# Optimization experiments

Hardware: AMD Instinct MI355X
Metric: run time of the kernel (lower is better)

The kernel has to match this reference:

```python
import jax, jax.numpy as jnp
import numpy as np

N_ROI = 262144
FEATURE_DIM = 256
HIDDEN_DIM = 64
N_NETWORKS = 128


def setup_inputs() -> dict:
    key = jax.random.key(0)
    ks = jax.random.split(key, 5)
    x = jax.random.normal(ks[0], (N_ROI, FEATURE_DIM), dtype=jnp.float32)
    group = jax.random.randint(ks[1], (N_ROI,), 0, N_NETWORKS, dtype=jnp.int32)
    W1 = jax.random.normal(ks[2], (FEATURE_DIM, HIDDEN_DIM), dtype=jnp.float32) / np.sqrt(FEATURE_DIM)
    b1 = jnp.zeros((HIDDEN_DIM,), dtype=jnp.float32)
    W2 = jax.random.normal(ks[3], (HIDDEN_DIM, 1), dtype=jnp.float32) / np.sqrt(HIDDEN_DIM)
    b2 = jnp.zeros((1,), dtype=jnp.float32)
    return {"x": x, "group": group, "W1": W1, "b1": b1, "W2": W2, "b2": b2}


def reference(x, group, W1, b1, W2, b2):
    # attention MLP score per ROI: Linear -> ReLU -> Linear(->1)
    h = jax.nn.relu(x @ W1 + b1)                       # [N, H]
    score = (h @ W2)[:, 0] + b2[0]                     # [N]
    # numerically-stable segment softmax over each network's ROIs
    seg_max = jax.ops.segment_max(score, group, num_segments=N_NETWORKS)  # [K]
    seg_max = jnp.where(jnp.isfinite(seg_max), seg_max, 0.0)              # empty segments -> 0
    w = jnp.exp(score - seg_max[group])                # [N] unnormalized weights
    denom = jax.ops.segment_sum(w, group, num_segments=N_NETWORKS)        # [K]
    num = jax.ops.segment_sum(w[:, None] * x, group, num_segments=N_NETWORKS)  # [K, D]
    # empty networks produce zeros (matches torch.zeros_like branch)
    return jnp.where(denom[:, None] > 0, num / jnp.maximum(denom, 1e-30)[:, None], 0.0)
```

## Files before the change

kernel.cpp:

```cpp
#include <hip/hip_runtime.h>
#include <hip/hip_bf16.h>

#define N_ROI 262144
#define FDIM  256
#define HDIM  64
#define NNET  128

#define TILE   128
#define TILES  8
#define RPB    (TILE * TILES)
#define NBLK   (N_ROI / RPB)
#define XPITCH 264

typedef __attribute__((ext_vector_type(8))) __bf16 bf16x8;
typedef __attribute__((ext_vector_type(8))) short short8;
typedef __attribute__((ext_vector_type(4))) float floatx4;

union frag_cast { short8 s; bf16x8 b; };

#define NEG_INF (-__builtin_huge_valf())

__device__ __forceinline__ unsigned fkey(float f) {
  unsigned u = __float_as_uint(f);
  return (u & 0x80000000u) ? ~u : (u | 0x80000000u);
}
__device__ __forceinline__ float fkey_inv(unsigned k) {
  unsigned u = (k & 0x80000000u) ? (k ^ 0x80000000u) : ~k;
  return __uint_as_float(u);
}
__device__ __forceinline__ unsigned short f2bf(float f) {
  unsigned u = __float_as_uint(f);
  u += 0x7FFFu + ((u >> 16) & 1u);
  return (unsigned short)(u >> 16);
}
__device__ __forceinline__ float bf2f(unsigned short h) {
  return __uint_as_float(((unsigned)h) << 16);
}
__device__ __forceinline__ unsigned cvt2(float a, float b) {
  union { __hip_bfloat162 h; unsigned u; } cv;
  cv.h = __float22bfloat162_rn(make_float2(a, b));
  return cv.u;
}

__global__ __launch_bounds__(512, 2) void fused_kernel(
    const float* __restrict__ x, const int* __restrict__ group,
    const float* __restrict__ W1, const float* __restrict__ b1,
    const float* __restrict__ W2,
    float* __restrict__ num_ws,
    float* __restrict__ m_ws)
{
  __shared__ __align__(16) unsigned short w1t[HDIM][XPITCH];
  __shared__ __align__(16) unsigned short xl[TILE][XPITCH];
  __shared__ float sc[TILE];
  __shared__ int   ggrp[TILE];
  __shared__ unsigned gw[TILE];
  __shared__ unsigned tmax[NNET];
  __shared__ __align__(16) float fl[NNET];
  __shared__ float mrun[NNET];
  __shared__ float dent[NNET];
  __shared__ float denrun[NNET];

  const int tid  = threadIdx.x;
  const int wave = tid >> 6, lane = tid & 63;
  const int col  = lane & 15, quad = lane >> 4;

  {
    const int n = tid & 63, kg = tid >> 6;
    for (int p = 0; p < 4; ++p) {
      const int k0 = p * 64 + kg * 8;
      unsigned short tmp[8];
#pragma unroll
      for (int j = 0; j < 8; ++j) tmp[j] = f2bf(W1[(k0 + j) * HDIM + n]);
      *(short8*)&w1t[n][k0] = *(short8*)tmp;
    }
  }
  if (tid < NNET) { mrun[tid] = NEG_INF; denrun[tid] = 0.f; }

  float b1v[4], w2v[4];
#pragma unroll
  for (int nt = 0; nt < 4; ++nt) { b1v[nt] = b1[nt * 16 + col]; w2v[nt] = W2[nt * 16 + col]; }

  floatx4 acc[8][2];
#pragma unroll
  for (int mt = 0; mt < 8; ++mt) { acc[mt][0] = (floatx4)0.f; acc[mt][1] = (floatx4)0.f; }

  const size_t rbase = (size_t)blockIdx.x * RPB;
  const float* xb = x + rbase * FDIM;

  float4 pf[16];
#pragma unroll
  for (int i = 0; i < 16; ++i)
    pf[i] = *(const float4*)(xb + i * 2048 + tid * 4);

  for (int t = 0; t < TILES; ++t) {
    __syncthreads();
#pragma unroll
    for (int i = 0; i < 16; ++i) {
      const int row = i * 8 + (tid >> 6);
      const int dim = (tid & 63) * 4;
      unsigned lo = cvt2(pf[i].x, pf[i].y);
      unsigned hi = cvt2(pf[i].z, pf[i].w);
      uint2 pk; pk.x = lo; pk.y = hi;
      *(uint2*)&xl[row][dim] = pk;
    }
    if (tid < TILE) {
      ggrp[tid] = group[rbase + t * TILE + tid];
      tmax[tid] = 0u;
      dent[tid] = 0.f;
    }
    __syncthreads();

    if (t < TILES - 1) {
      const float* xn = xb + (size_t)(t + 1) * TILE * FDIM;
#pragma unroll
      for (int i = 0; i < 16; ++i)
        pf[i] = *(const float4*)(xn + i * 2048 + tid * 4);
    }

    floatx4 accS[4];
#pragma unroll
    for (int nt = 0; nt < 4; ++nt) accS[nt] = (floatx4)0.f;
#pragma unroll
    for (int c = 0; c < 8; ++c) {
      frag_cast af;
      af.s = *(const short8*)&xl[wave * 16 + col][c * 32 + quad * 8];
#pragma unroll
      for (int nt = 0; nt < 4; ++nt) {
        frag_cast bf;
        bf.s = *(const short8*)&w1t[nt * 16 + col][c * 32 + quad * 8];
        accS[nt] = __builtin_amdgcn_mfma_f32_16x16x32_bf16(af.b, bf.b, accS[nt], 0, 0, 0);
      }
    }
    {
      float pr[4];
#pragma unroll
      for (int r = 0; r < 4; ++r) pr[r] = 0.f;
#pragma unroll
      for (int nt = 0; nt < 4; ++nt)
#pragma unroll
        for (int r = 0; r < 4; ++r)
          pr[r] += fmaxf(accS[nt][r] + b1v[nt], 0.f) * w2v[nt];
#pragma unroll
      for (int off = 1; off < 16; off <<= 1)
#pragma unroll
        for (int r = 0; r < 4; ++r) pr[r] += __shfl_xor(pr[r], off, 16);
      if (col == 0) {
#pragma unroll
        for (int r = 0; r < 4; ++r) sc[wave * 16 + quad * 4 + r] = pr[r];
      }
    }
    __syncthreads();

    if (tid < TILE) atomicMax(&tmax[ggrp[tid]], fkey(sc[tid]));
    __syncthreads();
    if (tid < NNET) {
      const unsigned tk = tmax[tid];
      float f = 1.f;
      if (tk) {
        const float mo = mrun[tid];
        const float mn = fmaxf(mo, fkey_inv(tk));
        f = __expf(mo - mn);
        mrun[tid] = mn;
      }
      fl[tid] = f;
    }
    __syncthreads();
    if (tid < TILE) {
      const int g = ggrp[tid];
      const float w = __expf(sc[tid] - mrun[g]);
      const unsigned short wb = f2bf(w);
      gw[tid] = ((unsigned)ggrp[tid] << 16) | wb;
      atomicAdd(&dent[g], bf2f(wb));
    }
#pragma unroll
    for (int mt = 0; mt < 8; ++mt) {
      const floatx4 f4 = *(const floatx4*)&fl[mt * 16 + quad * 4];
#pragma unroll
      for (int r = 0; r < 4; ++r) {
        acc[mt][0][r] *= f4[r];
        acc[mt][1][r] *= f4[r];
      }
    }
    __syncthreads();
    if (tid < NNET) denrun[tid] = denrun[tid] * fl[tid] + dent[tid];

    const int ntb = wave * 32;
#pragma unroll
    for (int c = 0; c < 4; ++c) {
      unsigned gwv[8];
#pragma unroll
      for (int j = 0; j < 8; ++j) gwv[j] = gw[c * 32 + quad * 8 + j];
      frag_cast bfx[2];
#pragma unroll
      for (int nt = 0; nt < 2; ++nt) {
        unsigned short bb[8];
#pragma unroll
        for (int j = 0; j < 8; ++j)
          bb[j] = xl[c * 32 + quad * 8 + j][ntb + nt * 16 + col];
        bfx[nt].s = *(short8*)bb;
      }
#pragma unroll
      for (int mt = 0; mt < 8; ++mt) {
        const unsigned gt = (unsigned)(mt * 16 + col);
        unsigned short aa[8];
#pragma unroll
        for (int j = 0; j < 8; ++j)
          aa[j] = ((gwv[j] >> 16) == gt) ? (unsigned short)gwv[j] : (unsigned short)0;
        frag_cast af; af.s = *(short8*)aa;
        acc[mt][0] = __builtin_amdgcn_mfma_f32_16x16x32_bf16(af.b, bfx[0].b, acc[mt][0], 0, 0, 0);
        acc[mt][1] = __builtin_amdgcn_mfma_f32_16x16x32_bf16(af.b, bfx[1].b, acc[mt][1], 0, 0, 0);
      }
    }
  }

  float* slice = num_ws + (size_t)blockIdx.x * (NNET * 257);
#pragma unroll
  for (int mt = 0; mt < 8; ++mt)
#pragma unroll
    for (int nt = 0; nt < 2; ++nt)
#pragma unroll
      for (int r = 0; r < 4; ++r)
        slice[(mt * 16 + quad * 4 + r) * 257 + wave * 32 + nt * 16 + col] = acc[mt][nt][r];
  if (tid < NNET) {
    slice[tid * 257 + 256] = denrun[tid];
    m_ws[(size_t)blockIdx.x * NNET + tid] = mrun[tid];
  }
}

__global__ __launch_bounds__(256) void finalize_kernel(
    const float* __restrict__ num_ws, const float* __restrict__ m_ws,
    float* __restrict__ out)
{
  const int g = blockIdx.x;
  const int tid = threadIdx.x;
  __shared__ float e_l[NBLK];
  __shared__ float dsum[NBLK];
  __shared__ float wm[4];

  const float mb = m_ws[(size_t)tid * NNET + g];
  float M = mb;
#pragma unroll
  for (int off = 1; off < 64; off <<= 1) M = fmaxf(M, __shfl_xor(M, off));
  if ((tid & 63) == 0) wm[tid >> 6] = M;
  __syncthreads();
  M = fmaxf(fmaxf(wm[0], wm[1]), fmaxf(wm[2], wm[3]));

  const float eb = (mb == NEG_INF) ? 0.f : __expf(mb - M);
  const float db = num_ws[(size_t)tid * (NNET * 257) + g * 257 + 256];
  e_l[tid]  = eb;
  dsum[tid] = db * eb;
  __syncthreads();

  float num = 0.f, den = 0.f;
#pragma unroll 4
  for (int b = 0; b < NBLK; ++b) {
    num += num_ws[(size_t)b * (NNET * 257) + g * 257 + tid] * e_l[b];
    den += dsum[b];
  }
  out[g * FDIM + tid] = (den > 0.f) ? num / fmaxf(den, 1e-30f) : 0.f;
}

extern "C" void kernel_launch(void* const* d_in, const int* in_sizes, int n_in,
                              void* d_out, int out_size, void* d_ws, size_t ws_size,
                              hipStream_t stream)
{
  const float* x     = (const float*)d_in[0];
  const int*   group = (const int*)d_in[1];
  const float* W1    = (const float*)d_in[2];
  const float* b1    = (const float*)d_in[3];
  const float* W2    = (const float*)d_in[4];
  float* out = (float*)d_out;

  float* num_ws = (float*)d_ws;
  float* m_ws   = num_ws + (size_t)NBLK * NNET * 257;

  fused_kernel<<<NBLK, 512, 0, stream>>>(x, group, W1, b1, W2, num_ws, m_ws);
  finalize_kernel<<<NNET, 256, 0, stream>>>(num_ws, m_ws, out);

  (void)in_sizes; (void)n_in; (void)out_size; (void)ws_size;
}
```

Measured before the change: 401.1 us.

## Restructure fused kernel to 256-thread blocks with 32-row chunks and swizzled LDS

The fused kernel now uses 256 threads per block over 512 rows in 16 chunks of 32. The first GEMM is split across waves by hidden column, with partial scores summed through shared memory. An XOR swizzle is applied to the x tile in LDS to reduce bank conflicts, and group ids are preloaded once per block. The block count doubles to 512, so the finalize kernel is split into two halves per network with a two-way block reduction. This trades more blocks and workspace traffic for lower per-block latency and better occupancy, but adds more barriers per row processed.

```diff
diff --git a/kernel.cpp b/kernel.cpp
--- a/kernel.cpp
+++ b/kernel.cpp
@@ -6,9 +6,9 @@
 #define HDIM  64
 #define NNET  128
 
-#define TILE   128
-#define TILES  8
-#define RPB    (TILE * TILES)
+#define CHUNK  32
+#define NCHUNK 16
+#define RPB    (CHUNK * NCHUNK)
 #define NBLK   (N_ROI / RPB)
 #define XPITCH 264
 
@@ -41,24 +41,26 @@
   cv.h = __float22bfloat162_rn(make_float2(a, b));
   return cv.u;
 }
-
-__global__ __launch_bounds__(512, 2) void fused_kernel(
+__device__ __forceinline__ int sidx(int row, int s) {
+  return row * XPITCH + (s ^ (((row >> 3) & 3) << 4));
+}
+
+__global__ __launch_bounds__(256, 2) void fused_kernel(
     const float* __restrict__ x, const int* __restrict__ group,
     const float* __restrict__ W1, const float* __restrict__ b1,
     const float* __restrict__ W2,
     float* __restrict__ num_ws,
     float* __restrict__ m_ws)
 {
-  __shared__ __align__(16) unsigned short w1t[HDIM][XPITCH];
-  __shared__ __align__(16) unsigned short xl[TILE][XPITCH];
-  __shared__ float sc[TILE];
-  __shared__ int   ggrp[TILE];
-  __shared__ unsigned gw[TILE];
+  __shared__ unsigned short w1t[HDIM][XPITCH];
+  __shared__ __align__(16) unsigned short xl[CHUNK * XPITCH];
+  __shared__ float scpart[4][CHUNK];
+  __shared__ float sc[CHUNK];
+  __shared__ int   ggrp[RPB];
+  __shared__ unsigned gw[CHUNK];
   __shared__ unsigned tmax[NNET];
   __shared__ __align__(16) float fl[NNET];
-  __shared__ float mrun[NNET];
-  __shared__ float dent[NNET];
-  __shared__ float denrun[NNET];
+  __shared__ float mrun[NNET], dent[NNET], denrun[NNET];
 
   const int tid  = threadIdx.x;
   const int wave = tid >> 6, lane = tid & 63;
@@ -66,8 +68,8 @@
 
   {
     const int n = tid & 63, kg = tid >> 6;
-    for (int p = 0; p < 4; ++p) {
-      const int k0 = p * 64 + kg * 8;
+    for (int p = 0; p < 8; ++p) {
+      const int k0 = p * 32 + kg * 8;
       unsigned short tmp[8];
 #pragma unroll
       for (int j = 0; j < 8; ++j) tmp[j] = f2bf(W1[(k0 + j) * HDIM + n]);
@@ -76,82 +78,77 @@
   }
   if (tid < NNET) { mrun[tid] = NEG_INF; denrun[tid] = 0.f; }
 
-  float b1v[4], w2v[4];
-#pragma unroll
-  for (int nt = 0; nt < 4; ++nt) { b1v[nt] = b1[nt * 16 + col]; w2v[nt] = W2[nt * 16 + col]; }
-
-  floatx4 acc[8][2];
-#pragma unroll
-  for (int mt = 0; mt < 8; ++mt) { acc[mt][0] = (floatx4)0.f; acc[mt][1] = (floatx4)0.f; }
-
   const size_t rbase = (size_t)blockIdx.x * RPB;
+  ggrp[tid]       = group[rbase + tid];
+  ggrp[tid + 256] = group[rbase + tid + 256];
+
+  const float b1s = b1[wave * 16 + col];
+  const float w2s = W2[wave * 16 + col];
+
+  floatx4 acc[8][4];
+#pragma unroll
+  for (int mt = 0; mt < 8; ++mt)
+#pragma unroll
+    for (int nt = 0; nt < 4; ++nt) acc[mt][nt] = (floatx4)0.f;
+
   const float* xb = x + rbase * FDIM;
 
-  float4 pf[16];
-#pragma unroll
-  for (int i = 0; i < 16; ++i)
-    pf[i] = *(const float4*)(xb + i * 2048 + tid * 4);
-
-  for (int t = 0; t < TILES; ++t) {
-    __syncthreads();
-#pragma unroll
-    for (int i = 0; i < 16; ++i) {
-      const int row = i * 8 + (tid >> 6);
-      const int dim = (tid & 63) * 4;
-      unsigned lo = cvt2(pf[i].x, pf[i].y);
-      unsigned hi = cvt2(pf[i].z, pf[i].w);
-      uint2 pk; pk.x = lo; pk.y = hi;
-      *(uint2*)&xl[row][dim] = pk;
-    }
-    if (tid < TILE) {
-      ggrp[tid] = group[rbase + t * TILE + tid];
-      tmax[tid] = 0u;
-      dent[tid] = 0.f;
-    }
-    __syncthreads();
-
-    if (t < TILES - 1) {
-      const float* xn = xb + (size_t)(t + 1) * TILE * FDIM;
-#pragma unroll
-      for (int i = 0; i < 16; ++i)
-        pf[i] = *(const float4*)(xn + i * 2048 + tid * 4);
-    }
-
-    floatx4 accS[4];
-#pragma unroll
-    for (int nt = 0; nt < 4; ++nt) accS[nt] = (floatx4)0.f;
+  float4 pf[8];
+#pragma unroll
+  for (int i = 0; i < 8; ++i)
+    pf[i] = *(const float4*)(xb + i * 1024 + tid * 4);
+
+  for (int ch = 0; ch < NCHUNK; ++ch) {
+    __syncthreads();
+#pragma unroll
+    for (int i = 0; i < 8; ++i) {
+      const int row = i * 4 + wave;
+      uint2 pk; pk.x = cvt2(pf[i].x, pf[i].y); pk.y = cvt2(pf[i].z, pf[i].w);
+      *(uint2*)&xl[sidx(row, lane * 4)] = pk;
+    }
+    if (tid < NNET) tmax[tid] = 0u;
+    __syncthreads();
+
+    if (ch < NCHUNK - 1) {
+      const float* xn = xb + (size_t)(ch + 1) * CHUNK * FDIM;
+#pragma unroll
+      for (int i = 0; i < 8; ++i)
+        pf[i] = *(const float4*)(xn + i * 1024 + tid * 4);
+    }
+
+    floatx4 accS[2];
+    accS[0] = (floatx4)0.f; accS[1] = (floatx4)0.f;
 #pragma unroll
     for (int c = 0; c < 8; ++c) {
-      frag_cast af;
-      af.s = *(const short8*)&xl[wave * 16 + col][c * 32 + quad * 8];
-#pragma unroll
-      for (int nt = 0; nt < 4; ++nt) {
-        frag_cast bf;
-        bf.s = *(const short8*)&w1t[nt * 16 + col][c * 32 + quad * 8];
-        accS[nt] = __builtin_amdgcn_mfma_f32_16x16x32_bf16(af.b, bf.b, accS[nt], 0, 0, 0);
+      frag_cast bw;
+      bw.s = *(const short8*)&w1t[wave * 16 + col][c * 32 + quad * 8];
+#pragma unroll
+      for (int mt = 0; mt < 2; ++mt) {
+        frag_cast af;
+        af.s = *(const short8*)&xl[sidx(mt * 16 + col, c * 32 + quad * 8)];
+        accS[mt] = __builtin_amdgcn_mfma_f32_16x16x32_bf16(af.b, bw.b, accS[mt], 0, 0, 0);
       }
     }
-    {
+#pragma unroll
+    for (int mt = 0; mt < 2; ++mt) {
       float pr[4];
 #pragma unroll
-      for (int r = 0; r < 4; ++r) pr[r] = 0.f;
-#pragma unroll
-      for (int nt = 0; nt < 4; ++nt)
-#pragma unroll
-        for (int r = 0; r < 4; ++r)
-          pr[r] += fmaxf(accS[nt][r] + b1v[nt], 0.f) * w2v[nt];
+      for (int r = 0; r < 4; ++r) pr[r] = fmaxf(accS[mt][r] + b1s, 0.f) * w2s;
 #pragma unroll
       for (int off = 1; off < 16; off <<= 1)
 #pragma unroll
         for (int r = 0; r < 4; ++r) pr[r] += __shfl_xor(pr[r], off, 16);
       if (col == 0) {
 #pragma unroll
-        for (int r = 0; r < 4; ++r) sc[wave * 16 + quad * 4 + r] = pr[r];
+        for (int r = 0; r < 4; ++r) scpart[wave][mt * 16 + quad * 4 + r] = pr[r];
       }
     }
     __syncthreads();
-
-    if (tid < TILE) atomicMax(&tmax[ggrp[tid]], fkey(sc[tid]));
+    if (tid < CHUNK) {
+      const float s = scpart[0][tid] + scpart[1][tid] + scpart[2][tid] + scpart[3][tid];
+      sc[tid] = s;
+      atomicMax(&tmax[ggrp[ch * CHUNK + tid]], fkey(s));
+    }
     __syncthreads();
     if (tid < NNET) {
       const unsigned tk = tmax[tid];
@@ -163,64 +160,61 @@
         mrun[tid] = mn;
       }
       fl[tid] = f;
-    }
-    __syncthreads();
-    if (tid < TILE) {
-      const int g = ggrp[tid];
+      dent[tid] = 0.f;
+    }
+    __syncthreads();
+    if (tid < CHUNK) {
+      const int g = ggrp[ch * CHUNK + tid];
       const float w = __expf(sc[tid] - mrun[g]);
       const unsigned short wb = f2bf(w);
-      gw[tid] = ((unsigned)ggrp[tid] << 16) | wb;
+      gw[tid] = ((unsigned)g << 16) | wb;
       atomicAdd(&dent[g], bf2f(wb));
     }
 #pragma unroll
     for (int mt = 0; mt < 8; ++mt) {
       const floatx4 f4 = *(const floatx4*)&fl[mt * 16 + quad * 4];
 #pragma unroll
-      for (int r = 0; r < 4; ++r) {
-        acc[mt][0][r] *= f4[r];
-        acc[mt][1][r] *= f4[r];
-      }
-    }
-    __syncthreads();
+      for (int nt = 0; nt < 4; ++nt)
+#pragma unroll
+        for (int r = 0; r < 4; ++r) acc[mt][nt][r] *= f4[r];
+    }
+    __syncthreads();
+
+    unsigned gwv[8];
+#pragma unroll
+    for (int j = 0; j < 8; ++j) gwv[j] = gw[quad * 8 + j];
+    frag_cast bfx[4];
+#pragma unroll
+    for (int nt = 0; nt < 4; ++nt) {
+      unsigned short bb[8];
+#pragma unroll
+      for (int j = 0; j < 8; ++j)
+        bb[j] = xl[sidx(quad * 8 + j, wave * 64 + nt * 16 + col)];
+      bfx[nt].s = *(short8*)bb;
+    }
+#pragma unroll
+    for (int mt = 0; mt < 8; ++mt) {
+      const unsigned gt = (unsigned)(mt * 16 + col);
+      unsigned short aa[8];
+#pragma unroll
+      for (int j = 0; j < 8; ++j)
+        aa[j] = ((gwv[j] >> 16) == gt) ? (unsigned short)gwv[j] : (unsigned short)0;
+      frag_cast af; af.s = *(short8*)aa;
+#pragma unroll
+      for (int nt = 0; nt < 4; ++nt)
+        acc[mt][nt] = __builtin_amdgcn_mfma_f32_16x16x32_bf16(af.b, bfx[nt].b, acc[mt][nt], 0, 0, 0);
+    }
     if (tid < NNET) denrun[tid] = denrun[tid] * fl[tid] + dent[tid];
-
-    const int ntb = wave * 32;
-#pragma unroll
-    for (int c = 0; c < 4; ++c) {
-      unsigned gwv[8];
-#pragma unroll
-      for (int j = 0; j < 8; ++j) gwv[j] = gw[c * 32 + quad * 8 + j];
-      frag_cast bfx[2];
-#pragma unroll
-      for (int nt = 0; nt < 2; ++nt) {
-        unsigned short bb[8];
-#pragma unroll
-        for (int j = 0; j < 8; ++j)
-          bb[j] = xl[c * 32 + quad * 8 + j][ntb + nt * 16 + col];
-        bfx[nt].s = *(short8*)bb;
-      }
-#pragma unroll
-      for (int mt = 0; mt < 8; ++mt) {
-        const unsigned gt = (unsigned)(mt * 16 + col);
-        unsigned short aa[8];
-#pragma unroll
-        for (int j = 0; j < 8; ++j)
-          aa[j] = ((gwv[j] >> 16) == gt) ? (unsigned short)gwv[j] : (unsigned short)0;
-        frag_cast af; af.s = *(short8*)aa;
-        acc[mt][0] = __builtin_amdgcn_mfma_f32_16x16x32_bf16(af.b, bfx[0].b, acc[mt][0], 0, 0, 0);
-        acc[mt][1] = __builtin_amdgcn_mfma_f32_16x16x32_bf16(af.b, bfx[1].b, acc[mt][1], 0, 0, 0);
-      }
-    }
   }
 
   float* slice = num_ws + (size_t)blockIdx.x * (NNET * 257);
 #pragma unroll
   for (int mt = 0; mt < 8; ++mt)
 #pragma unroll
-    for (int nt = 0; nt < 2; ++nt)
+    for (int nt = 0; nt < 4; ++nt)
 #pragma unroll
       for (int r = 0; r < 4; ++r)
-        slice[(mt * 16 + quad * 4 + r) * 257 + wave * 32 + nt * 16 + col] = acc[mt][nt][r];
+        slice[(mt * 16 + quad * 4 + r) * 257 + wave * 64 + nt * 16 + col] = acc[mt][nt][r];
   if (tid < NNET) {
     slice[tid * 257 + 256] = denrun[tid];
     m_ws[(size_t)blockIdx.x * NNET + tid] = mrun[tid];
@@ -231,33 +225,47 @@
     const float* __restrict__ num_ws, const float* __restrict__ m_ws,
     float* __restrict__ out)
 {
-  const int g = blockIdx.x;
-  const int tid = threadIdx.x;
+  const int g     = blockIdx.x >> 1;
+  const int dbase = (blockIdx.x & 1) << 7;
+  const int tid   = threadIdx.x;
   __shared__ float e_l[NBLK];
-  __shared__ float dsum[NBLK];
-  __shared__ float wm[4];
-
-  const float mb = m_ws[(size_t)tid * NNET + g];
-  float M = mb;
+  __shared__ float red[8];
+  __shared__ float npart[2][128];
+
+  const float m0 = m_ws[(size_t)tid * NNET + g];
+  const float m1 = m_ws[(size_t)(tid + 256) * NNET + g];
+  float M = fmaxf(m0, m1);
 #pragma unroll
   for (int off = 1; off < 64; off <<= 1) M = fmaxf(M, __shfl_xor(M, off));
-  if ((tid & 63) == 0) wm[tid >> 6] = M;
+  if ((tid & 63) == 0) red[tid >> 6] = M;
   __syncthreads();
-  M = fmaxf(fmaxf(wm[0], wm[1]), fmaxf(wm[2], wm[3]));
-
-  const float eb = (mb == NEG_INF) ? 0.f : __expf(mb - M);
-  const float db = num_ws[(size_t)tid * (NNET * 257) + g * 257 + 256];
-  e_l[tid]  = eb;
-  dsum[tid] = db * eb;
+  M = fmaxf(fmaxf(red[0], red[1]), fmaxf(red[2], red[3]));
+
+  const float e0 = (m0 == NEG_INF) ? 0.f : __expf(m0 - M);
+  const float e1 = (m1 == NEG_INF) ? 0.f : __expf(m1 - M);
+  e_l[tid]       = e0;
+  e_l[tid + 256] = e1;
+  float dp = num_ws[(size_t)tid * (NNET * 257) + g * 257 + 256] * e0
+           + num_ws[(size_t)(tid + 256) * (NNET * 257) + g * 257 + 256] * e1;
+#pragma unroll
+  for (int off = 1; off < 64; off <<= 1) dp += __shfl_xor(dp, off);
+  if ((tid & 63) == 0) red[4 + (tid >> 6)] = dp;
   __syncthreads();
-
-  float num = 0.f, den = 0.f;
+  const float den = red[4] + red[5] + red[6] + red[7];
+
+  const int dd = tid & 127, half = tid >> 7;
+  float nsum = 0.f;
+  const float* base = num_ws + (size_t)half * 256 * (NNET * 257) + g * 257 + dbase + dd;
+  const float* el   = e_l + half * 256;
 #pragma unroll 4
-  for (int b = 0; b < NBLK; ++b) {
-    num += num_ws[(size_t)b * (NNET * 257) + g * 257 + tid] * e_l[b];
-    den += dsum[b];
-  }
-  out[g * FDIM + tid] = (den > 0.f) ? num / fmaxf(den, 1e-30f) : 0.f;
+  for (int b = 0; b < 256; ++b)
+    nsum += base[(size_t)b * (NNET * 257)] * el[b];
+  npart[half][dd] = nsum;
+  __syncthreads();
+  if (tid < 128) {
+    const float num = npart[0][tid] + npart[1][tid];
+    out[g * FDIM + dbase + tid] = (den > 0.f) ? num / fmaxf(den, 1e-30f) : 0.f;
+  }
 }
 
 extern "C" void kernel_launch(void* const* d_in, const int* in_sizes, int n_in,
@@ -274,8 +282,8 @@
   float* num_ws = (float*)d_ws;
   float* m_ws   = num_ws + (size_t)NBLK * NNET * 257;
 
-  fused_kernel<<<NBLK, 512, 0, stream>>>(x, group, W1, b1, W2, num_ws, m_ws);
-  finalize_kernel<<<NNET, 256, 0, stream>>>(num_ws, m_ws, out);
+  fused_kernel<<<NBLK, 256, 0, stream>>>(x, group, W1, b1, W2, num_ws, m_ws);
+  finalize_kernel<<<2 * NNET, 256, 0, stream>>>(num_ws, m_ws, out);
 
   (void)in_sizes; (void)n_in; (void)out_size; (void)ws_size;
 }
```

Result: slower. 429.0 us (+7.0%).
